# Kernel optimization log

Measured on AMD Instinct MI355X. Metric: run time of the kernel, lower is better.

## Reference

```python
import jax, jax.numpy as jnp
import numpy as np

K = 3
KK = K * K


def _conv1x1(x, w, b):
    # x: [B,Ci,H,W], w: [Co,Ci]
    return jnp.einsum('bihw,oi->bohw', x, w) + b[None, :, None, None]


def _conv3x3(x, w, b):
    y = jax.lax.conv_general_dilated(x, w, (1, 1), ((1, 1), (1, 1)),
                                     dimension_numbers=('NCHW', 'OIHW', 'NCHW'))
    return y + b[None, :, None, None]


def _deform_conv3x3(x, offset, w, b):
    # Deformable conv v1, kernel 3x3, stride 1, pad 1, dilation 1, 1 deformable group.
    # x: [B,C,H,W]; offset: [B,2*KK,H,W] (dy,dx interleaved per kernel tap); w: [Co,C,3,3]
    B, C, H, W = x.shape
    dt = x.dtype
    off = offset.reshape(B, KK, 2, H, W)
    ky, kx = jnp.meshgrid(jnp.arange(K, dtype=dt), jnp.arange(K, dtype=dt), indexing='ij')
    ky = ky.reshape(KK)
    kx = kx.reshape(KK)
    # sampling locations: out_pos - pad + kernel_tap + learned offset
    base_y = jnp.arange(H, dtype=dt) - 1.0  # pad = 1
    base_x = jnp.arange(W, dtype=dt) - 1.0
    sy = base_y[None, None, :, None] + ky[None, :, None, None] + off[:, :, 0]  # [B,KK,H,W]
    sx = base_x[None, None, None, :] + kx[None, :, None, None] + off[:, :, 1]
    y0 = jnp.floor(sy)
    x0 = jnp.floor(sx)
    ty = sy - y0
    tx = sx - x0

    def gather(iy, ix):
        valid = ((iy >= 0) & (iy <= H - 1) & (ix >= 0) & (ix <= W - 1)).astype(dt)
        iyc = jnp.clip(iy, 0, H - 1).astype(jnp.int32)
        ixc = jnp.clip(ix, 0, W - 1).astype(jnp.int32)
        vals = jax.vmap(lambda img, a, c: img[:, a, c])(x, iyc, ixc)  # [B,C,KK,H,W]
        return vals * valid[:, None]

    w00 = ((1 - ty) * (1 - tx))[:, None]
    w01 = ((1 - ty) * tx)[:, None]
    w10 = (ty * (1 - tx))[:, None]
    w11 = (ty * tx)[:, None]
    sampled = (gather(y0, x0) * w00 + gather(y0, x0 + 1) * w01 +
               gather(y0 + 1, x0) * w10 + gather(y0 + 1, x0 + 1) * w11)  # [B,C,KK,H,W]
    Co = w.shape[0]
    out = jnp.einsum('bikhw,oik->bohw', sampled, w.reshape(Co, C, KK))
    return out + b[None, :, None, None]


def _branch(features, dw, db, ow, ob, tw, tb):
    h = _conv1x1(features, dw, db)
    off = _conv3x3(h, ow, ob)  # offset-predicting conv inside DFConv2d
    return jax.nn.relu(_deform_conv3x3(h, off, tw, tb))


def setup_inputs() -> dict:
    key = jax.random.key(0)
    ks = jax.random.split(key, 13)
    C = 256
    s1 = 1.0 / np.sqrt(C)          # kaiming_normal a=1 for 1x1 conv
    s3 = 1.0 / np.sqrt(C * KK)     # 3x3 conv
    so = 0.01                       # small offset-conv weights -> modest offsets
    f = lambda k, s, sc: jax.random.normal(k, s, dtype=jnp.float32) * sc
    return {
        'features': f(ks[0], (4, C, 64, 64), 1.0),
        'agg_down_w': f(ks[1], (C, C), s1),
        'agg_down_b': jnp.zeros((C,), jnp.float32),
        'agg_off_w': f(ks[2], (2 * KK, C, K, K), so),
        'agg_off_b': jnp.zeros((2 * KK,), jnp.float32),
        'agg_w': f(ks[3], (C, C, K, K), s3),
        'agg_b': jnp.zeros((C,), jnp.float32),
        'appr_down_w': f(ks[4], (C, C), s1),
        'appr_down_b': jnp.zeros((C,), jnp.float32),
        'appr_off_w': f(ks[5], (2 * KK, C, K, K), so),
        'appr_off_b': jnp.zeros((2 * KK,), jnp.float32),
        'appr_w': f(ks[6], (C, C, K, K), s3),
        'appr_b': jnp.zeros((C,), jnp.float32),
    }


def reference(features, agg_down_w, agg_down_b, agg_off_w, agg_off_b, agg_w, agg_b,
              appr_down_w, appr_down_b, appr_off_w, appr_off_b, appr_w, appr_b):
    agg = _branch(features, agg_down_w, agg_down_b, agg_off_w, agg_off_b, agg_w, agg_b)
    appr = _branch(features, appr_down_w, appr_down_b, appr_off_w, appr_off_b, appr_w, appr_b)
    return (agg, appr)
```

## Files before the change

kernel.cpp:

```cpp
#include <hip/hip_runtime.h>

#define HWP 4096
#define NPIX 4194304
#define KDIM 2304

typedef __attribute__((ext_vector_type(4))) float f32x4;
typedef __attribute__((ext_vector_type(4))) int   i32x4;
typedef __attribute__((ext_vector_type(8))) short short8;
typedef __attribute__((ext_vector_type(4))) unsigned short bf16x4;
typedef __attribute__((ext_vector_type(4))) unsigned short u16x4;

__device__ __forceinline__ unsigned short bf16_rne(float f) {
    unsigned int u = __builtin_bit_cast(unsigned int, f);
    u += 0x7FFFu + ((u >> 16) & 1u);
    return (unsigned short)(u >> 16);
}

__device__ __forceinline__ float bf2f(unsigned short u) {
    return __builtin_bit_cast(float, (unsigned int)u << 16);
}

__device__ __forceinline__ float u2f_lo(unsigned int u) {
    return __builtin_bit_cast(float, u << 16);
}

__device__ __forceinline__ float u2f_hi(unsigned int u) {
    return __builtin_bit_cast(float, u & 0xFFFF0000u);
}

__device__ __forceinline__ unsigned int cvt_pk_bf16(float lo, float hi) {
    unsigned int r;
    asm("v_cvt_pk_bf16_f32 %0, %1, %2" : "=v"(r) : "v"(lo), "v"(hi));
    return r;
}

__device__ __forceinline__ void gload_lds16(const void* g, void* l) {
    __builtin_amdgcn_global_load_lds((const __attribute__((address_space(1))) void*)g,
                                     (__attribute__((address_space(3))) void*)l, 16, 0, 0);
}

__global__ void prep_all_kernel(const float* __restrict__ x, unsigned short* __restrict__ fbt,
                                const float* __restrict__ dw0, const float* __restrict__ dw1,
                                const float* __restrict__ tw0, const float* __restrict__ tw1,
                                const float* __restrict__ ow0, const float* __restrict__ ow1,
                                unsigned short* __restrict__ w1b2,
                                unsigned short* __restrict__ w2A,
                                unsigned short* __restrict__ w2o) {
    __shared__ float T[64][65];
    int b = blockIdx.x;
    int t = threadIdx.x;
    if (b < 1024) {
        int pt = b & 63, ct = (b >> 6) & 3, bb = b >> 8;
        int lane = t & 63;
        int r = t >> 6;
        int c0 = ct * 64, p0 = pt * 64;
        const float* xb = x + (size_t)(bb * 256 + c0) * HWP + p0;
#pragma unroll
        for (int rr = 0; rr < 16; ++rr) {
            int ci = r * 16 + rr;
            T[ci][lane] = xb[(size_t)ci * HWP + lane];
        }
        __syncthreads();
        unsigned short* ob = fbt + ((size_t)bb * HWP + p0) * 256 + c0;
#pragma unroll
        for (int rr = 0; rr < 16; ++rr) {
            int px = r * 16 + rr;
            ob[(size_t)px * 256 + lane] = bf16_rne(T[lane][px]);
        }
        return;
    }
    int idx = (b - 1024) * 256 + t;
    if (idx < 131072) {
        int br = idx >> 16;
        int i  = idx & 65535;
        const float* dw = br ? dw1 : dw0;
        w1b2[idx] = bf16_rne(dw[i]);
    } else if (idx < 131072 + 1179648) {
        int j = idx - 131072;
        int br = j >= 589824;
        int i  = br ? j - 589824 : j;
        const float* tw = br ? tw1 : tw0;
        int ci = i & 255;
        int r  = i >> 8;
        int tap = r % 9;
        int o   = r / 9;
        w2A[j] = bf16_rne(tw[(o * 256 + ci) * 9 + tap]);
    } else {
        int j = idx - 131072 - 1179648;
        int br = j >= 73728;
        int i  = br ? j - 73728 : j;
        const float* ow = br ? ow1 : ow0;
        int m = i / 2304;
        int k = i - m * 2304;
        int tap = k >> 8;
        int ci  = k & 255;
        w2o[j] = (m < 18) ? bf16_rne(ow[(m * 256 + ci) * 9 + tap]) : (unsigned short)0;
    }
}

__global__ void prep_w2_kernel(const float* __restrict__ tw0, const float* __restrict__ tw1,
                               unsigned short* __restrict__ w2) {
    int idx = blockIdx.x * 256 + threadIdx.x;
    int br = idx >= 589824;
    int i  = br ? idx - 589824 : idx;
    const float* tw = br ? tw1 : tw0;
    int ci = i & 255;
    int r  = i >> 8;
    int tap = r % 9;
    int o   = r / 9;
    w2[idx] = bf16_rne(tw[(o * 256 + ci) * 9 + tap]);
}

__global__ void prep_ow2_kernel(const float* __restrict__ ow0, const float* __restrict__ ow1,
                                float* __restrict__ owt) {
    int idx = blockIdx.x * 256 + threadIdx.x;
    int br = idx >= 41472;
    int i  = br ? idx - 41472 : idx;
    const float* ow = br ? ow1 : ow0;
    int co = i % 18;
    int r  = i / 18;
    int k  = r % 9;
    int ci = r / 9;
    owt[idx] = ow[(co * 256 + ci) * 9 + k];
}

__global__ void prep_w12_kernel(const float* __restrict__ dw0, const float* __restrict__ dw1,
                                unsigned short* __restrict__ w1b) {
    int idx = blockIdx.x * 256 + threadIdx.x;
    int br = idx >> 16;
    int i  = idx & 65535;
    const float* dw = br ? dw1 : dw0;
    w1b[idx] = bf16_rne(dw[i]);
}

__global__ void prep_fb16_kernel(const float* __restrict__ x, unsigned short* __restrict__ fbt) {
    __shared__ float T[64][65];
    int pt = blockIdx.x;
    int ct = blockIdx.y;
    int bb = blockIdx.z;
    int t = threadIdx.x;
    int lane = t & 63;
    int r = t >> 6;
    int c0 = ct * 64, p0 = pt * 64;
    const float* xb = x + (size_t)(bb * 256 + c0) * HWP + p0;
#pragma unroll
    for (int rr = 0; rr < 16; ++rr) {
        int ci = r * 16 + rr;
        T[ci][lane] = xb[(size_t)ci * HWP + lane];
    }
    __syncthreads();
    unsigned short* ob = fbt + ((size_t)bb * HWP + p0) * 256 + c0;
#pragma unroll
    for (int rr = 0; rr < 16; ++rr) {
        int px = r * 16 + rr;
        ob[(size_t)px * 256 + lane] = bf16_rne(T[lane][px]);
    }
}

__launch_bounds__(256)
__global__ void gemm1x1_kernel(const unsigned short* __restrict__ w1b2,
                               const unsigned short* __restrict__ fbt,
                               const float* __restrict__ db0, const float* __restrict__ db1,
                               float* __restrict__ h2, unsigned short* __restrict__ ht2,
                               int write_h) {
    __shared__ unsigned short As[128 * 64];
    __shared__ unsigned short Bs[64 * 64];
    int pt = blockIdx.x;
    int ot = blockIdx.y;
    int z  = blockIdx.z;
    int bb = z & 3;
    int br = z >> 2;
    const unsigned short* w1b = w1b2 + (size_t)br * 65536;
    const float* db = br ? db1 : db0;
    int t  = threadIdx.x;
    int l  = t & 63;
    int w  = t >> 6;
    int wr = w >> 1, wc = w & 1;
    int o0 = ot * 128, p0 = pt * 64;
    const unsigned short* fb = fbt + (size_t)bb * HWP * 256;
    f32x4 acc[4][2];
#pragma unroll
    for (int i = 0; i < 4; ++i)
#pragma unroll
        for (int j = 0; j < 2; ++j) acc[i][j] = (f32x4){0.f, 0.f, 0.f, 0.f};

    for (int ks = 0; ks < 4; ++ks) {
        int k0 = ks * 64;
#pragma unroll
        for (int rA = 0; rA < 4; ++rA) {
            int s = rA * 256 + t;
            int row = s >> 3, cg = (s & 7) ^ (row & 7);
            gload_lds16(w1b + (size_t)(o0 + row) * 256 + k0 + cg * 8, As + s * 8);
        }
#pragma unroll
        for (int rB = 0; rB < 2; ++rB) {
            int s = rB * 256 + t;
            int row = s >> 3, cg = (s & 7) ^ (row & 7);
            gload_lds16(fb + (size_t)(p0 + row) * 256 + k0 + cg * 8, Bs + s * 8);
        }
        __syncthreads();
#pragma unroll
        for (int half = 0; half < 2; ++half) {
            short8 a[4], b[2];
#pragma unroll
            for (int fr = 0; fr < 4; ++fr) {
                int row = wr * 64 + fr * 16 + (l & 15);
                int oct = half * 4 + (l >> 4);
                a[fr] = *reinterpret_cast<const short8*>(As + row * 64 + ((oct ^ (row & 7)) * 8));
            }
#pragma unroll
            for (int fc = 0; fc < 2; ++fc) {
                int row = wc * 32 + fc * 16 + (l & 15);
                int oct = half * 4 + (l >> 4);
                b[fc] = *reinterpret_cast<const short8*>(Bs + row * 64 + ((oct ^ (row & 7)) * 8));
            }
#pragma unroll
            for (int fr = 0; fr < 4; ++fr)
#pragma unroll
                for (int fc = 0; fc < 2; ++fc)
                    acc[fr][fc] = __builtin_amdgcn_mfma_f32_16x16x32_bf16(a[fr], b[fc], acc[fr][fc], 0, 0, 0);
        }
        __syncthreads();
    }

    float* hb = h2 + (size_t)br * NPIX + (size_t)bb * 256 * HWP;
    unsigned short* htb = ht2 + (size_t)br * NPIX + (size_t)bb * HWP * 256;
#pragma unroll
    for (int fr = 0; fr < 4; ++fr) {
        int o = o0 + wr * 64 + fr * 16 + ((l >> 4) << 2);
#pragma unroll
        for (int fc = 0; fc < 2; ++fc) {
            int p = p0 + wc * 32 + fc * 16 + (l & 15);
            f32x4 v;
#pragma unroll
            for (int reg = 0; reg < 4; ++reg) {
                v[reg] = acc[fr][fc][reg] + db[o + reg];
                if (write_h) hb[(size_t)(o + reg) * HWP + p] = v[reg];
            }
            uint2 pk;
            pk.x = cvt_pk_bf16(v[0], v[1]);
            pk.y = cvt_pk_bf16(v[2], v[3]);
            *reinterpret_cast<uint2*>(htb + (size_t)p * 256 + o) = pk;
        }
    }
}

__launch_bounds__(256)
__global__ void off_mfma_kernel(const unsigned short* __restrict__ w2o,
                                const unsigned short* __restrict__ ht2,
                                const float* __restrict__ ob0, const float* __restrict__ ob1,
                                float* __restrict__ dwq, unsigned short* __restrict__ dcq) {
    __shared__ float red[4][1152];
    int id = blockIdx.x;
    int br = id >> 8;
    int bb = (id >> 6) & 3;
    int y  = id & 63;
    const unsigned short* wA = w2o + (size_t)br * 73728;
    const unsigned short* htb = ht2 + (size_t)br * NPIX + (size_t)bb * HWP * 256;
    const float* ob = br ? ob1 : ob0;
    int t = threadIdx.x;
    int l = t & 63;
    int w = t >> 6;
    short8 zero = {};
    f32x4 acc[2][4];
#pragma unroll
    for (int i = 0; i < 2; ++i)
#pragma unroll
        for (int j = 0; j < 4; ++j) acc[i][j] = (f32x4){0.f, 0.f, 0.f, 0.f};

    for (int tap = 0; tap < 9; ++tap) {
        int ky = tap / 3, kx = tap % 3;
        int yy = y + ky - 1;
        bool vy = (yy >= 0) && (yy < 64);
        int cyy = min(max(yy, 0), 63);
#pragma unroll
        for (int sh = 0; sh < 2; ++sh) {
            int s = w * 2 + sh;
            short8 a[2], b[4];
#pragma unroll
            for (int fr = 0; fr < 2; ++fr)
                a[fr] = *reinterpret_cast<const short8*>(
                    wA + (size_t)(fr * 16 + (l & 15)) * KDIM + tap * 256 + s * 32 + ((l >> 4) << 3));
#pragma unroll
            for (int fc = 0; fc < 4; ++fc) {
                int px = fc * 16 + (l & 15);
                int xx = px + kx - 1;
                bool v = vy && (xx >= 0) && (xx < 64);
                int cxx = min(max(xx, 0), 63);
                short8 bv = *reinterpret_cast<const short8*>(
                    htb + (size_t)(cyy * 64 + cxx) * 256 + s * 32 + ((l >> 4) << 3));
                b[fc] = v ? bv : zero;
            }
#pragma unroll
            for (int fr = 0; fr < 2; ++fr)
#pragma unroll
                for (int fc = 0; fc < 4; ++fc)
                    acc[fr][fc] = __builtin_amdgcn_mfma_f32_16x16x32_bf16(a[fr], b[fc], acc[fr][fc], 0, 0, 0);
        }
    }

#pragma unroll
    for (int fr = 0; fr < 2; ++fr)
#pragma unroll
        for (int fc = 0; fc < 4; ++fc) {
            int px = fc * 16 + (l & 15);
#pragma unroll
            for (int reg = 0; reg < 4; ++reg) {
                int co = fr * 16 + ((l >> 4) << 2) + reg;
                if (co < 18) red[w][co * 64 + px] = acc[fr][fc][reg];
            }
        }
    __syncthreads();

    size_t dbase = ((size_t)(br * 4 + bb) * 9) * 4096 + (size_t)(y * 64);
    for (int e = t; e < 576; e += 256) {
        int tap = e >> 6, px = e & 63;
        int c0 = 2 * tap, c1 = 2 * tap + 1;
        float dy = ob[c0] + red[0][c0 * 64 + px] + red[1][c0 * 64 + px]
                          + red[2][c0 * 64 + px] + red[3][c0 * 64 + px];
        float dx = ob[c1] + red[0][c1 * 64 + px] + red[1][c1 * 64 + px]
                          + red[2][c1 * 64 + px] + red[3][c1 * 64 + px];
        int ky = tap / 3, kx = tap % 3;
        float sy = (float)(y - 1 + ky) + dy;
        float sx = (float)(px - 1 + kx) + dx;
        float y0f = floorf(sy), x0f = floorf(sx);
        float ty = sy - y0f, tx = sx - x0f;
        int iy0 = (int)y0f, ix0 = (int)x0f;
        int iy1 = iy0 + 1, ix1 = ix0 + 1;
        bool vy0 = (iy0 >= 0) & (iy0 < 64);
        bool vy1 = (iy1 >= 0) & (iy1 < 64);
        bool vx0 = (ix0 >= 0) & (ix0 < 64);
        bool vx1 = (ix1 >= 0) & (ix1 < 64);
        int cy0 = min(max(iy0, 0), 63), cy1 = min(max(iy1, 0), 63);
        int cx0 = min(max(ix0, 0), 63), cx1 = min(max(ix1, 0), 63);
        f32x4 ww;
        ww[0] = (1.f - ty) * (1.f - tx) * ((vy0 & vx0) ? 1.f : 0.f);
        ww[1] = (1.f - ty) * tx * ((vy0 & vx1) ? 1.f : 0.f);
        ww[2] = ty * (1.f - tx) * ((vy1 & vx0) ? 1.f : 0.f);
        ww[3] = ty * tx * ((vy1 & vx1) ? 1.f : 0.f);
        u16x4 pc;
        pc[0] = (unsigned short)(cy0 * 64 + cx0);
        pc[1] = (unsigned short)(cy0 * 64 + cx1);
        pc[2] = (unsigned short)(cy1 * 64 + cx0);
        pc[3] = (unsigned short)(cy1 * 64 + cx1);
        size_t di = dbase + (size_t)tap * 4096 + px;
        *reinterpret_cast<f32x4*>(dwq + di * 4) = ww;
        *reinterpret_cast<u16x4*>(dcq + di * 4) = pc;
    }
}

__global__ void off_conv_part_kernel(const float* __restrict__ h2, const float* __restrict__ owt2,
                                     float* __restrict__ part2) {
    int y  = blockIdx.x & 63;
    int bb = blockIdx.x >> 6;
    int c  = blockIdx.y;
    int br = blockIdx.z;
    const float* h = h2 + (size_t)br * NPIX;
    const float* owt = owt2 + (size_t)br * 41472;
    float* part = part2 + (size_t)br * 2359296;
    int t  = threadIdx.x;
    int x  = t & 63;
    int wv = __builtin_amdgcn_readfirstlane(t >> 6);
    int  toff[9];
    bool tval[9];
#pragma unroll
    for (int ky = 0; ky < 3; ++ky) {
        int yy = y + ky - 1;
        bool vy = (yy >= 0) && (yy < 64);
        int cyy = min(max(yy, 0), 63);
#pragma unroll
        for (int kx = 0; kx < 3; ++kx) {
            int xx = x + kx - 1;
            tval[ky * 3 + kx] = vy && (xx >= 0) && (xx < 64);
            toff[ky * 3 + kx] = cyy * 64 + min(max(xx, 0), 63);
        }
    }
    float acc[18];
#pragma unroll
    for (int co = 0; co < 18; ++co) acc[co] = 0.f;
    int ci0 = c * 32 + wv * 8;
    const float* hb = h + (size_t)(bb * 256 + ci0) * HWP;
#pragma unroll
    for (int i = 0; i < 8; ++i) {
        const float* hc = hb + i * HWP;
        const float* wci = owt + (size_t)(ci0 + i) * 162;
#pragma unroll
        for (int k = 0; k < 9; ++k) {
            float hv = hc[toff[k]];
            hv = tval[k] ? hv : 0.f;
            const float* wk = wci + k * 18;
#pragma unroll
            for (int co = 0; co < 18; ++co)
                acc[co] = fmaf(wk[co], hv, acc[co]);
        }
    }
    __shared__ float red[4][18][64];
    int wvl = t >> 6;
#pragma unroll
    for (int co = 0; co < 18; ++co) red[wvl][co][x] = acc[co];
    __syncthreads();
    if (wvl == 0) {
#pragma unroll
        for (int co = 0; co < 18; ++co) {
            float s = red[0][co][x] + red[1][co][x] + red[2][co][x] + red[3][co][x];
            part[(size_t)c * 294912 + ((bb * 18 + co) << 12) + (y << 6) + x] = s;
        }
    }
}

__global__ void off_reduce2_kernel(const float* __restrict__ part2,
                                   const float* __restrict__ ob0, const float* __restrict__ ob1,
                                   float* __restrict__ off2) {
    int idx = blockIdx.x * 256 + threadIdx.x;
    int br = idx >= 294912;
    int i  = br ? idx - 294912 : idx;
    const float* part = part2 + (size_t)br * 2359296;
    const float* b = br ? ob1 : ob0;
    int co = (i >> 12) % 18;
    float s = b[co];
#pragma unroll
    for (int c = 0; c < 8; ++c) s += part[(size_t)c * 294912 + i];
    off2[idx] = s;
}

__launch_bounds__(512, 4)
__global__ void dgemm_fused_kernel(const unsigned short* __restrict__ w2b,
                                   const unsigned short* __restrict__ ht2,
                                   const float* __restrict__ dwq,
                                   const unsigned short* __restrict__ dcq,
                                   const float* __restrict__ tb0,
                                   const float* __restrict__ tb1,
                                   float* __restrict__ out) {
    __shared__ unsigned short As[2][8][1024];
    __shared__ unsigned short Bs[64 * 256];
    int id = blockIdx.x;
    int sw = (id & 7) * 64 + (id >> 3);
    int br = sw >> 8;
    int mt = sw & 255;
    int bb = mt >> 6;
    int y  = mt & 63;
    const unsigned short* w2 = w2b + (size_t)br * 589824;
    const unsigned short* htb = ht2 + (size_t)br * NPIX + (size_t)bb * HWP * 256;
    const float* bias = br ? tb1 : tb0;
    size_t dbase = ((size_t)(br * 4 + bb) * 9) * 4096 + (size_t)(y * 64);
    int t = threadIdx.x;
    int l = t & 63;
    int w = t >> 6;
    int wvu = __builtin_amdgcn_readfirstlane(w);
    int le = l << 2;

    f32x4 acc[2][4];
#pragma unroll
    for (int i = 0; i < 2; ++i)
#pragma unroll
        for (int j = 0; j < 4; ++j) acc[i][j] = (f32x4){0.f, 0.f, 0.f, 0.f};

#define STAGE_AS(buf, ss)                                                          \
    do {                                                                           \
        _Pragma("unroll")                                                          \
        for (int r_ = 0; r_ < 2; ++r_) {                                           \
            int idx_ = r_ * 64 + l;                                                \
            int row_ = idx_ >> 2;                                                  \
            int kc_ = (idx_ & 3) ^ ((row_ >> 1) & 3);                              \
            gload_lds16(wtap + (size_t)(wvu * 32 + row_) * KDIM + (ss) * 32 + kc_ * 8, \
                        &As[buf][wvu][idx_ * 8]);                                  \
        }                                                                          \
    } while (0)

    for (int tap = 0; tap < 9; ++tap) {
        const unsigned short* wtap = w2 + tap * 256;
        const float* dwt = dwq + (dbase + (size_t)tap * 4096) * 4;
        const unsigned short* dct = dcq + (dbase + (size_t)tap * 4096) * 4;
        __syncthreads();
        STAGE_AS(0, 0);
#pragma unroll
        for (int i = 0; i < 8; ++i) {
            int px = wvu * 8 + i;
            f32x4 ww = *reinterpret_cast<const f32x4*>(dwt + (size_t)px * 4);
            u16x4 pc = *reinterpret_cast<const u16x4*>(dct + (size_t)px * 4);
            int b00 = ((int)pc[0] << 8) + le;
            int b01 = ((int)pc[1] << 8) + le;
            int b10 = ((int)pc[2] << 8) + le;
            int b11 = ((int)pc[3] << 8) + le;
            uint2 u00 = *reinterpret_cast<const uint2*>(htb + b00);
            uint2 u01 = *reinterpret_cast<const uint2*>(htb + b01);
            uint2 u10 = *reinterpret_cast<const uint2*>(htb + b10);
            uint2 u11 = *reinterpret_cast<const uint2*>(htb + b11);
            float s0 = fmaf(ww[0], u2f_lo(u00.x),
                       fmaf(ww[1], u2f_lo(u01.x),
                       fmaf(ww[2], u2f_lo(u10.x), ww[3] * u2f_lo(u11.x))));
            float s1 = fmaf(ww[0], u2f_hi(u00.x),
                       fmaf(ww[1], u2f_hi(u01.x),
                       fmaf(ww[2], u2f_hi(u10.x), ww[3] * u2f_hi(u11.x))));
            float s2 = fmaf(ww[0], u2f_lo(u00.y),
                       fmaf(ww[1], u2f_lo(u01.y),
                       fmaf(ww[2], u2f_lo(u10.y), ww[3] * u2f_lo(u11.y))));
            float s3 = fmaf(ww[0], u2f_hi(u00.y),
                       fmaf(ww[1], u2f_hi(u01.y),
                       fmaf(ww[2], u2f_hi(u10.y), ww[3] * u2f_hi(u11.y))));
            uint2 pk;
            pk.x = cvt_pk_bf16(s0, s1);
            pk.y = cvt_pk_bf16(s2, s3);
            int g = l >> 1, sub = l & 1;
            *reinterpret_cast<uint2*>(Bs + px * 256 + (((g ^ (px & 7)) << 3) | (sub << 2))) = pk;
        }
        __syncthreads();
        for (int s = 0; s < 8; ++s) {
            if (s < 7) {
                int buf = (s + 1) & 1;
                STAGE_AS(buf, s + 1);
            }
            asm volatile("s_waitcnt vmcnt(2)" ::: "memory");
            __builtin_amdgcn_sched_barrier(0);
            short8 a[2], b[4];
#pragma unroll
            for (int fr = 0; fr < 2; ++fr) {
                int rowl = fr * 16 + (l & 15);
                int oct = (l >> 4) ^ ((rowl >> 1) & 3);
                a[fr] = *reinterpret_cast<const short8*>(&As[s & 1][wvu][rowl * 32 + oct * 8]);
            }
#pragma unroll
            for (int fc = 0; fc < 4; ++fc) {
                int prow = fc * 16 + (l & 15);
                int cg8 = (s << 2) + (l >> 4);
                b[fc] = *reinterpret_cast<const short8*>(Bs + prow * 256 + ((cg8 ^ (prow & 7)) << 3));
            }
            __builtin_amdgcn_s_setprio(1);
#pragma unroll
            for (int fr = 0; fr < 2; ++fr)
#pragma unroll
                for (int fc = 0; fc < 4; ++fc)
                    acc[fr][fc] = __builtin_amdgcn_mfma_f32_16x16x32_bf16(a[fr], b[fc], acc[fr][fc], 0, 0, 0);
            __builtin_amdgcn_s_setprio(0);
        }
    }
#undef STAGE_AS

    float* outp = out + (size_t)br * NPIX + (size_t)(bb * 256) * HWP + y * 64;
#pragma unroll
    for (int fr = 0; fr < 2; ++fr) {
        int o = w * 32 + fr * 16 + ((l >> 4) << 2);
#pragma unroll
        for (int fc = 0; fc < 4; ++fc) {
            int pxc = fc * 16 + (l & 15);
#pragma unroll
            for (int reg = 0; reg < 4; ++reg) {
                float v = acc[fr][fc][reg] + bias[o + reg];
                outp[(size_t)(o + reg) * HWP + pxc] = fmaxf(v, 0.f);
            }
        }
    }
}

__launch_bounds__(256)
__global__ void sample2_kernel(const unsigned short* __restrict__ ht, const float* __restrict__ off,
                               unsigned short* __restrict__ sm, int b0) {
    int y   = blockIdx.x;
    int tap = blockIdx.y;
    int bb  = b0 + blockIdx.z;
    int t   = threadIdx.x;
    int lane = t & 63;
    int wv  = t >> 6;
    int ky = tap / 3, kx = tap % 3;
    const unsigned short* htb = ht + (size_t)bb * HWP * 256;
    const float* offy = off + ((bb * 18 + 2 * tap) * 64 + y) * 64;
    const float* offx = off + ((bb * 18 + 2 * tap + 1) * 64 + y) * 64;
    int mrow = ((bb - b0) * 64 + y) * 64;
#pragma unroll 4
    for (int i = 0; i < 16; ++i) {
        int px = wv * 16 + i;
        float dy = offy[px];
        float dx = offx[px];
        float sy = (float)(y - 1 + ky) + dy;
        float sx = (float)(px - 1 + kx) + dx;
        float y0f = floorf(sy), x0f = floorf(sx);
        float ty = sy - y0f, tx = sx - x0f;
        int iy0 = (int)y0f, ix0 = (int)x0f;
        int iy1 = iy0 + 1, ix1 = ix0 + 1;
        bool vy0 = (iy0 >= 0) & (iy0 < 64);
        bool vy1 = (iy1 >= 0) & (iy1 < 64);
        bool vx0 = (ix0 >= 0) & (ix0 < 64);
        bool vx1 = (ix1 >= 0) & (ix1 < 64);
        int cy0 = min(max(iy0, 0), 63), cy1 = min(max(iy1, 0), 63);
        int cx0 = min(max(ix0, 0), 63), cx1 = min(max(ix1, 0), 63);
        float w00 = (1.f - ty) * (1.f - tx) * ((vy0 & vx0) ? 1.f : 0.f);
        float w01 = (1.f - ty) * tx * ((vy0 & vx1) ? 1.f : 0.f);
        float w10 = ty * (1.f - tx) * ((vy1 & vx0) ? 1.f : 0.f);
        float w11 = ty * tx * ((vy1 & vx1) ? 1.f : 0.f);
        int le = lane << 2;
        bf16x4 q00 = *reinterpret_cast<const bf16x4*>(htb + ((cy0 * 64 + cx0) << 8) + le);
        bf16x4 q01 = *reinterpret_cast<const bf16x4*>(htb + ((cy0 * 64 + cx1) << 8) + le);
        bf16x4 q10 = *reinterpret_cast<const bf16x4*>(htb + ((cy1 * 64 + cx0) << 8) + le);
        bf16x4 q11 = *reinterpret_cast<const bf16x4*>(htb + ((cy1 * 64 + cx1) << 8) + le);
        f32x4 s;
#pragma unroll
        for (int j = 0; j < 4; ++j)
            s[j] = fmaf(w00, bf2f(q00[j]),
                   fmaf(w01, bf2f(q01[j]),
                   fmaf(w10, bf2f(q10[j]), w11 * bf2f(q11[j]))));
        uint2 pk;
        pk.x = cvt_pk_bf16(s[0], s[1]);
        pk.y = cvt_pk_bf16(s[2], s[3]);
        *reinterpret_cast<uint2*>(sm + (size_t)(mrow + px) * KDIM + tap * 256 + lane * 4) = pk;
    }
}

__launch_bounds__(256)
__global__ void gemm2_kernel(const unsigned short* __restrict__ w2b,
                             const unsigned short* __restrict__ smb, size_t smstride,
                             const float* __restrict__ tb0, const float* __restrict__ tb1,
                             float* __restrict__ out, int mbase) {
    __shared__ unsigned short As[128 * 64];
    __shared__ unsigned short Bs[64 * 64];
    int mt = blockIdx.x;
    int ot = blockIdx.y;
    int br = blockIdx.z;
    const unsigned short* w2 = w2b + (size_t)br * 589824;
    const unsigned short* sm = smb + (size_t)br * smstride;
    const float* bias = br ? tb1 : tb0;
    float* outp = out + (size_t)br * NPIX;
    int t  = threadIdx.x;
    int l  = t & 63;
    int w  = t >> 6;
    int wr = w >> 1, wc = w & 1;
    int o0 = ot * 128, m0 = mt * 64;
    f32x4 acc[4][2];
#pragma unroll
    for (int i = 0; i < 4; ++i)
#pragma unroll
        for (int j = 0; j < 2; ++j) acc[i][j] = (f32x4){0.f, 0.f, 0.f, 0.f};

    for (int ks = 0; ks < KDIM / 64; ++ks) {
        int k0 = ks * 64;
#pragma unroll
        for (int rA = 0; rA < 4; ++rA) {
            int s = rA * 256 + t;
            int row = s >> 3, cg = (s & 7) ^ (row & 7);
            gload_lds16(w2 + (size_t)(o0 + row) * KDIM + k0 + cg * 8, As + s * 8);
        }
#pragma unroll
        for (int rB = 0; rB < 2; ++rB) {
            int s = rB * 256 + t;
            int row = s >> 3, cg = (s & 7) ^ (row & 7);
            gload_lds16(sm + (size_t)(m0 + row) * KDIM + k0 + cg * 8, Bs + s * 8);
        }
        __syncthreads();
#pragma unroll
        for (int half = 0; half < 2; ++half) {
            short8 a[4], b[2];
#pragma unroll
            for (int fr = 0; fr < 4; ++fr) {
                int row = wr * 64 + fr * 16 + (l & 15);
                int oct = half * 4 + (l >> 4);
                a[fr] = *reinterpret_cast<const short8*>(As + row * 64 + ((oct ^ (row & 7)) * 8));
            }
#pragma unroll
            for (int fc = 0; fc < 2; ++fc) {
                int row = wc * 32 + fc * 16 + (l & 15);
                int oct = half * 4 + (l >> 4);
                b[fc] = *reinterpret_cast<const short8*>(Bs + row * 64 + ((oct ^ (row & 7)) * 8));
            }
#pragma unroll
            for (int fr = 0; fr < 4; ++fr)
#pragma unroll
                for (int fc = 0; fc < 2; ++fc)
                    acc[fr][fc] = __builtin_amdgcn_mfma_f32_16x16x32_bf16(a[fr], b[fc], acc[fr][fc], 0, 0, 0);
        }
        __syncthreads();
    }

#pragma unroll
    for (int fr = 0; fr < 4; ++fr) {
        int o = o0 + wr * 64 + fr * 16 + ((l >> 4) << 2);
#pragma unroll
        for (int fc = 0; fc < 2; ++fc) {
            int mg = mbase + m0 + wc * 32 + fc * 16 + (l & 15);
            int bbv = mg >> 12;
            int pix = mg & 4095;
            float* op = outp + (size_t)(bbv * 256) * HWP + pix;
#pragma unroll
            for (int reg = 0; reg < 4; ++reg) {
                float v = acc[fr][fc][reg] + bias[o + reg];
                op[(size_t)(o + reg) * HWP] = fmaxf(v, 0.f);
            }
        }
    }
}

extern "C" void kernel_launch(void* const* d_in, const int* in_sizes, int n_in,
                              void* d_out, int out_size, void* d_ws, size_t ws_size,
                              hipStream_t stream) {
    const float* feat = (const float*)d_in[0];
    char* base = (char*)d_ws;
    float* outp = (float*)d_out;
    const size_t perb = (size_t)HWP * KDIM * 2;

    const float* dw0 = (const float*)d_in[1];
    const float* db0 = (const float*)d_in[2];
    const float* ow0 = (const float*)d_in[3];
    const float* ob0 = (const float*)d_in[4];
    const float* tw0 = (const float*)d_in[5];
    const float* tb0 = (const float*)d_in[6];
    const float* dw1 = (const float*)d_in[7];
    const float* db1 = (const float*)d_in[8];
    const float* ow1 = (const float*)d_in[9];
    const float* ob1 = (const float*)d_in[10];
    const float* tw1 = (const float*)d_in[11];
    const float* tb1 = (const float*)d_in[12];

    bool tierA = ws_size >= 47218688;

    if (tierA) {
        unsigned short* ht2 = (unsigned short*)base;
        unsigned short* w2A = (unsigned short*)(base + 35913728);
        unsigned short* w2o = (unsigned short*)(base + 38273024);
        unsigned short* fbt = (unsigned short*)(base + 38567936);
        unsigned short* w1b2 = (unsigned short*)(base + 46956544);
        float* dwq = (float*)(base + 38567936);
        unsigned short* dcq = (unsigned short*)(base + 38567936 + 4718592);

        hipLaunchKernelGGL(prep_all_kernel, dim3(6720), dim3(256), 0, stream,
                           feat, fbt, dw0, dw1, tw0, tw1, ow0, ow1, w1b2, w2A, w2o);
        hipLaunchKernelGGL(gemm1x1_kernel, dim3(64, 2, 8), dim3(256), 0, stream,
                           w1b2, fbt, db0, db1, (float*)nullptr, ht2, 0);
        hipLaunchKernelGGL(off_mfma_kernel, dim3(512), dim3(256), 0, stream,
                           w2o, ht2, ob0, ob1, dwq, dcq);
        hipLaunchKernelGGL(dgemm_fused_kernel, dim3(512), dim3(512), 0, stream,
                           w2A, ht2, dwq, dcq, tb0, tb1, outp);
        return;
    }

    float* h   = (float*)base;
    float* off = h + NPIX;
    unsigned short* w2 = (unsigned short*)(base + 17956864);
    float* owt = (float*)(base + 19136512);
    unsigned short* ht = (unsigned short*)(base + 19302400);
    unsigned short* smN = (unsigned short*)(base + 27691008);
    float* partN = (float*)(base + 27691008);
    unsigned short* fbtN = (unsigned short*)(base + 27691008 + 9437184);
    unsigned short* w1bN = (unsigned short*)(base + 27691008 + 17825792);

    int nb = 0;
    if (27691008 + 4 * perb <= ws_size) nb = 4;
    else if (27691008 + 2 * perb <= ws_size) nb = 2;
    else nb = 1;

    for (int br = 0; br < 2; ++br) {
        const float* dw = (const float*)d_in[1 + 6 * br];
        const float* db = (const float*)d_in[2 + 6 * br];
        const float* ow = (const float*)d_in[3 + 6 * br];
        const float* ob = (const float*)d_in[4 + 6 * br];
        const float* tw = (const float*)d_in[5 + 6 * br];
        const float* tb = (const float*)d_in[6 + 6 * br];

        hipLaunchKernelGGL(prep_fb16_kernel, dim3(64, 4, 4), dim3(256), 0, stream, feat, fbtN);
        hipLaunchKernelGGL(prep_w12_kernel, dim3(256), dim3(256), 0, stream, dw, dw, w1bN);
        hipLaunchKernelGGL(gemm1x1_kernel, dim3(64, 2, 4), dim3(256), 0, stream,
                           w1bN, fbtN, db, db, h, ht, 1);
        hipLaunchKernelGGL(prep_ow2_kernel, dim3(162), dim3(256), 0, stream, ow, ow, owt);
        hipLaunchKernelGGL(off_conv_part_kernel, dim3(256, 8, 1), dim3(256), 0, stream,
                           h, owt, partN);
        hipLaunchKernelGGL(off_reduce2_kernel, dim3(1152), dim3(256), 0, stream,
                           partN, ob, ob, off);
        hipLaunchKernelGGL(prep_w2_kernel, dim3(2304), dim3(256), 0, stream, tw, tw, w2);

        for (int b0 = 0; b0 < 4; b0 += nb) {
            hipLaunchKernelGGL(sample2_kernel, dim3(64, 9, nb), dim3(256), 0, stream,
                               ht, off, smN, b0);
            hipLaunchKernelGGL(gemm2_kernel, dim3(nb * 64, 2, 1), dim3(256), 0, stream,
                               w2, smN, (size_t)0, tb, tb, outp + br * NPIX, b0 * HWP);
        }
    }
}
```

Measured before the change: 127.0 us.

## Load deform-GEMM weights directly into MFMA fragments and double-buffer sampled tile

Pre-permutes the deformable-conv weights into an MFMA fragment-native layout so each wave loads A operands straight from global memory into registers. This drops the LDS staging of A and its waitcnt barriers. The block shrinks from 512 to 256 threads, so each wave now covers 64 output channels with a 4x4 accumulator tile. The bilinearly sampled B tile is double-buffered in LDS, so sampling for the next tap overlaps with the MFMA work of the current tap. In exchange it uses more registers and each wave does more sampling work, and the A loads from global/L2 may stall the MFMAs.

After: 122.1 us. 3.9% less time.

```diff
diff --git a/kernel.cpp b/kernel.cpp
--- a/kernel.cpp
+++ b/kernel.cpp
@@ -80,10 +80,16 @@
         int br = j >= 589824;
         int i  = br ? j - 589824 : j;
         const float* tw = br ? tw1 : tw0;
-        int ci = i & 255;
-        int r  = i >> 8;
-        int tap = r % 9;
-        int o   = r / 9;
+        int cg = i / 147456;
+        int r  = i - cg * 147456;
+        int tap = r >> 14;
+        int r2 = r & 16383;
+        int s  = r2 >> 11;
+        int fr = (r2 >> 9) & 3;
+        int l  = (r2 >> 3) & 63;
+        int e  = r2 & 7;
+        int o  = cg * 64 + fr * 16 + (l & 15);
+        int ci = s * 32 + ((l >> 4) << 3) + e;
         w2A[j] = bf16_rne(tw[(o * 256 + ci) * 9 + tap]);
     } else {
         int j = idx - 131072 - 1179648;
@@ -423,7 +429,7 @@
     off2[idx] = s;
 }
 
-__launch_bounds__(512, 4)
+__launch_bounds__(256, 2)
 __global__ void dgemm_fused_kernel(const unsigned short* __restrict__ w2b,
                                    const unsigned short* __restrict__ ht2,
                                    const float* __restrict__ dwq,
@@ -431,15 +437,14 @@
                                    const float* __restrict__ tb0,
                                    const float* __restrict__ tb1,
                                    float* __restrict__ out) {
-    __shared__ unsigned short As[2][8][1024];
-    __shared__ unsigned short Bs[64 * 256];
+    __shared__ unsigned short Bs[2][64 * 256];
     int id = blockIdx.x;
     int sw = (id & 7) * 64 + (id >> 3);
     int br = sw >> 8;
     int mt = sw & 255;
     int bb = mt >> 6;
     int y  = mt & 63;
-    const unsigned short* w2 = w2b + (size_t)br * 589824;
+    const unsigned short* w2f = w2b + (size_t)br * 589824;
     const unsigned short* htb = ht2 + (size_t)br * NPIX + (size_t)bb * HWP * 256;
     const float* bias = br ? tb1 : tb0;
     size_t dbase = ((size_t)(br * 4 + bb) * 9) * 4096 + (size_t)(y * 64);
@@ -449,97 +454,112 @@
     int wvu = __builtin_amdgcn_readfirstlane(w);
     int le = l << 2;
 
-    f32x4 acc[2][4];
-#pragma unroll
-    for (int i = 0; i < 2; ++i)
+    f32x4 acc[4][4];
+#pragma unroll
+    for (int i = 0; i < 4; ++i)
 #pragma unroll
         for (int j = 0; j < 4; ++j) acc[i][j] = (f32x4){0.f, 0.f, 0.f, 0.f};
 
-#define STAGE_AS(buf, ss)                                                          \
+#define STAGE_B(TAPV, WB)                                                          \
     do {                                                                           \
+        const float* dwt = dwq + (dbase + (size_t)(TAPV) * 4096) * 4;              \
+        const unsigned short* dct = dcq + (dbase + (size_t)(TAPV) * 4096) * 4;     \
         _Pragma("unroll")                                                          \
-        for (int r_ = 0; r_ < 2; ++r_) {                                           \
-            int idx_ = r_ * 64 + l;                                                \
-            int row_ = idx_ >> 2;                                                  \
-            int kc_ = (idx_ & 3) ^ ((row_ >> 1) & 3);                              \
-            gload_lds16(wtap + (size_t)(wvu * 32 + row_) * KDIM + (ss) * 32 + kc_ * 8, \
-                        &As[buf][wvu][idx_ * 8]);                                  \
+        for (int i_ = 0; i_ < 16; ++i_) {                                          \
+            int px = wvu * 16 + i_;                                                \
+            f32x4 ww = *reinterpret_cast<const f32x4*>(dwt + (size_t)px * 4);      \
+            u16x4 pc = *reinterpret_cast<const u16x4*>(dct + (size_t)px * 4);      \
+            int b00 = ((int)pc[0] << 8) + le;                                      \
+            int b01 = ((int)pc[1] << 8) + le;                                      \
+            int b10 = ((int)pc[2] << 8) + le;                                      \
+            int b11 = ((int)pc[3] << 8) + le;                                      \
+            uint2 u00 = *reinterpret_cast<const uint2*>(htb + b00);                \
+            uint2 u01 = *reinterpret_cast<const uint2*>(htb + b01);                \
+            uint2 u10 = *reinterpret_cast<const uint2*>(htb + b10);                \
+            uint2 u11 = *reinterpret_cast<const uint2*>(htb + b11);                \
+            float s0 = fmaf(ww[0], u2f_lo(u00.x),                                  \
+                       fmaf(ww[1], u2f_lo(u01.x),                                  \
+                       fmaf(ww[2], u2f_lo(u10.x), ww[3] * u2f_lo(u11.x))));        \
+            float s1 = fmaf(ww[0], u2f_hi(u00.x),                                  \
+                       fmaf(ww[1], u2f_hi(u01.x),                                  \
+                       fmaf(ww[2], u2f_hi(u10.x), ww[3] * u2f_hi(u11.x))));        \
+            float s2 = fmaf(ww[0], u2f_lo(u00.y),                                  \
+                       fmaf(ww[1], u2f_lo(u01.y),                                  \
+                       fmaf(ww[2], u2f_lo(u10.y), ww[3] * u2f_lo(u11.y))));        \
+            float s3 = fmaf(ww[0], u2f_hi(u00.y),                                  \
+                       fmaf(ww[1], u2f_hi(u01.y),                                  \
+                       fmaf(ww[2], u2f_hi(u10.y), ww[3] * u2f_hi(u11.y))));        \
+            uint2 pk;                                                              \
+            pk.x = cvt_pk_bf16(s0, s1);                                            \
+            pk.y = cvt_pk_bf16(s2, s3);                                            \
+            int g = l >> 1, sub = l & 1;                                           \
+            *reinterpret_cast<uint2*>((WB) + px * 256 +                            \
+                (((g ^ (px & 7)) << 3) | (sub << 2))) = pk;                        \
         }                                                                          \
     } while (0)
 
-    for (int tap = 0; tap < 9; ++tap) {
-        const unsigned short* wtap = w2 + tap * 256;
-        const float* dwt = dwq + (dbase + (size_t)tap * 4096) * 4;
-        const unsigned short* dct = dcq + (dbase + (size_t)tap * 4096) * 4;
+#define COMPUTE_TAP(TAPV, RB)                                                      \
+    do {                                                                           \
+        const unsigned short* wtapf = w2f + (size_t)(wvu * 9 + (TAPV)) * 16384;    \
+        short8 aA[4], aB[4];                                                       \
+        _Pragma("unroll")                                                          \
+        for (int fr = 0; fr < 4; ++fr)                                             \
+            aA[fr] = *reinterpret_cast<const short8*>(wtapf + fr * 512 + (l << 3));\
+        _Pragma("unroll")                                                          \
+        for (int fr = 0; fr < 4; ++fr)                                             \
+            aB[fr] = *reinterpret_cast<const short8*>(wtapf + (4 + fr) * 512 + (l << 3)); \
+        _Pragma("unroll")                                                          \
+        for (int s = 0; s < 8; ++s) {                                              \
+            short8 aC[4];                                                          \
+            if (s < 6) {                                                           \
+                _Pragma("unroll")                                                  \
+                for (int fr = 0; fr < 4; ++fr)                                     \
+                    aC[fr] = *reinterpret_cast<const short8*>(                     \
+                        wtapf + (size_t)((s + 2) * 4 + fr) * 512 + (l << 3));      \
+            }                                                                      \
+            short8 b[4];                                                           \
+            _Pragma("unroll")                                                      \
+            for (int fc = 0; fc < 4; ++fc) {                                       \
+                int prow = fc * 16 + (l & 15);                                     \
+                int cg8 = (s << 2) + (l >> 4);                                     \
+                b[fc] = *reinterpret_cast<const short8*>(                          \
+                    (RB) + prow * 256 + ((cg8 ^ (prow & 7)) << 3));                \
+            }                                                                      \
+            __builtin_amdgcn_s_setprio(1);                                         \
+            _Pragma("unroll")                                                      \
+            for (int fr = 0; fr < 4; ++fr)                                         \
+                _Pragma("unroll")                                                  \
+                for (int fc = 0; fc < 4; ++fc)                                     \
+                    acc[fr][fc] = __builtin_amdgcn_mfma_f32_16x16x32_bf16(         \
+                        aA[fr], b[fc], acc[fr][fc], 0, 0, 0);                      \
+            __builtin_amdgcn_s_setprio(0);                                         \
+            if (s < 7) {                                                           \
+                _Pragma("unroll")                                                  \
+                for (int fr = 0; fr < 4; ++fr) { aA[fr] = aB[fr]; aB[fr] = aC[fr]; } \
+            }                                                                      \
+        }                                                                          \
+    } while (0)
+
+    STAGE_B(0, Bs[0]);
+    __syncthreads();
+#pragma unroll 1
+    for (int it = 0; it < 4; ++it) {
+        int tap = it * 2;
+        COMPUTE_TAP(tap, Bs[0]);
+        STAGE_B(tap + 1, Bs[1]);
         __syncthreads();
-        STAGE_AS(0, 0);
-#pragma unroll
-        for (int i = 0; i < 8; ++i) {
-            int px = wvu * 8 + i;
-            f32x4 ww = *reinterpret_cast<const f32x4*>(dwt + (size_t)px * 4);
-            u16x4 pc = *reinterpret_cast<const u16x4*>(dct + (size_t)px * 4);
-            int b00 = ((int)pc[0] << 8) + le;
-            int b01 = ((int)pc[1] << 8) + le;
-            int b10 = ((int)pc[2] << 8) + le;
-            int b11 = ((int)pc[3] << 8) + le;
-            uint2 u00 = *reinterpret_cast<const uint2*>(htb + b00);
-            uint2 u01 = *reinterpret_cast<const uint2*>(htb + b01);
-            uint2 u10 = *reinterpret_cast<const uint2*>(htb + b10);
-            uint2 u11 = *reinterpret_cast<const uint2*>(htb + b11);
-            float s0 = fmaf(ww[0], u2f_lo(u00.x),
-                       fmaf(ww[1], u2f_lo(u01.x),
-                       fmaf(ww[2], u2f_lo(u10.x), ww[3] * u2f_lo(u11.x))));
-            float s1 = fmaf(ww[0], u2f_hi(u00.x),
-                       fmaf(ww[1], u2f_hi(u01.x),
-                       fmaf(ww[2], u2f_hi(u10.x), ww[3] * u2f_hi(u11.x))));
-            float s2 = fmaf(ww[0], u2f_lo(u00.y),
-                       fmaf(ww[1], u2f_lo(u01.y),
-                       fmaf(ww[2], u2f_lo(u10.y), ww[3] * u2f_lo(u11.y))));
-            float s3 = fmaf(ww[0], u2f_hi(u00.y),
-                       fmaf(ww[1], u2f_hi(u01.y),
-                       fmaf(ww[2], u2f_hi(u10.y), ww[3] * u2f_hi(u11.y))));
-            uint2 pk;
-            pk.x = cvt_pk_bf16(s0, s1);
-            pk.y = cvt_pk_bf16(s2, s3);
-            int g = l >> 1, sub = l & 1;
-            *reinterpret_cast<uint2*>(Bs + px * 256 + (((g ^ (px & 7)) << 3) | (sub << 2))) = pk;
-        }
+        COMPUTE_TAP(tap + 1, Bs[1]);
+        STAGE_B(tap + 2, Bs[0]);
         __syncthreads();
-        for (int s = 0; s < 8; ++s) {
-            if (s < 7) {
-                int buf = (s + 1) & 1;
-                STAGE_AS(buf, s + 1);
-            }
-            asm volatile("s_waitcnt vmcnt(2)" ::: "memory");
-            __builtin_amdgcn_sched_barrier(0);
-            short8 a[2], b[4];
-#pragma unroll
-            for (int fr = 0; fr < 2; ++fr) {
-                int rowl = fr * 16 + (l & 15);
-                int oct = (l >> 4) ^ ((rowl >> 1) & 3);
-                a[fr] = *reinterpret_cast<const short8*>(&As[s & 1][wvu][rowl * 32 + oct * 8]);
-            }
-#pragma unroll
-            for (int fc = 0; fc < 4; ++fc) {
-                int prow = fc * 16 + (l & 15);
-                int cg8 = (s << 2) + (l >> 4);
-                b[fc] = *reinterpret_cast<const short8*>(Bs + prow * 256 + ((cg8 ^ (prow & 7)) << 3));
-            }
-            __builtin_amdgcn_s_setprio(1);
-#pragma unroll
-            for (int fr = 0; fr < 2; ++fr)
-#pragma unroll
-                for (int fc = 0; fc < 4; ++fc)
-                    acc[fr][fc] = __builtin_amdgcn_mfma_f32_16x16x32_bf16(a[fr], b[fc], acc[fr][fc], 0, 0, 0);
-            __builtin_amdgcn_s_setprio(0);
-        }
-    }
-#undef STAGE_AS
+    }
+    COMPUTE_TAP(8, Bs[0]);
+#undef STAGE_B
+#undef COMPUTE_TAP
 
     float* outp = out + (size_t)br * NPIX + (size_t)(bb * 256) * HWP + y * 64;
 #pragma unroll
-    for (int fr = 0; fr < 2; ++fr) {
-        int o = w * 32 + fr * 16 + ((l >> 4) << 2);
+    for (int fr = 0; fr < 4; ++fr) {
+        int o = wvu * 64 + fr * 16 + ((l >> 4) << 2);
 #pragma unroll
         for (int fc = 0; fc < 4; ++fc) {
             int pxc = fc * 16 + (l & 15);
@@ -725,7 +745,7 @@
                            w1b2, fbt, db0, db1, (float*)nullptr, ht2, 0);
         hipLaunchKernelGGL(off_mfma_kernel, dim3(512), dim3(256), 0, stream,
                            w2o, ht2, ob0, ob1, dwq, dcq);
-        hipLaunchKernelGGL(dgemm_fused_kernel, dim3(512), dim3(512), 0, stream,
+        hipLaunchKernelGGL(dgemm_fused_kernel, dim3(512), dim3(256), 0, stream,
                            w2A, ht2, dwq, dcq, tb0, tb1, outp);
         return;
     }
```
